# Optimization experiments

Hardware: AMD Instinct MI355X
Metric: run time of the kernel (lower is better)

Reference implementation:

```python
import jax, jax.numpy as jnp
import numpy as np

EPS = 1e-8


def setup_inputs() -> dict:
    key = jax.random.key(0)
    k1, k2 = jax.random.split(key)
    N, F, K, C = 16384, 64, 32, 100
    membership = jax.random.uniform(k1, (N, F, K), dtype=jnp.float32)
    teacher_probs = jax.random.uniform(k2, (N, C), dtype=jnp.float32)
    return {"membership": membership, "teacher_probs": teacher_probs}


def reference(membership, teacher_probs):
    # membership: [N, F, K]  soft bin assignments per feature
    # teacher_probs: [N, C]  teacher class distribution per sample
    N, F, K = membership.shape
    bin_mass = membership.sum(axis=0) + EPS  # [F, K]
    # Contraction form of (membership[:, :, :, None] * teacher_probs[:, None, None, :]).sum(0)
    # avoids the N*F*K*C intermediate.
    centroids = jnp.einsum('nfk,nc->fkc', membership, teacher_probs) / bin_mass[:, :, None]  # [F, K, C]
    # Intra-bin: minimize entropy of each bin's class distribution, mass-weighted.
    intra_entropy = -jnp.sum(centroids * jnp.log(centroids + EPS), axis=2)  # [F, K]
    loss_intra = jnp.sum(intra_entropy * bin_mass) / N
    # Inter-bin: maximize entropy of the mixture of adjacent bins
    # (loss_inter is negative entropy summed, added with +0.5 weight).
    mixture = 0.5 * (centroids[:, :-1, :] + centroids[:, 1:, :])  # [F, K-1, C]
    loss_inter = jnp.sum(mixture * jnp.log(mixture + EPS))
    return loss_intra + 0.5 * loss_inter
```

## Files before the change

kernel.cpp:

```cpp
#include <hip/hip_runtime.h>
#include <hip/hip_bf16.h>

#define NS   16384
#define FKD  2048
#define CD   100
#define CP   112
#define MT   64
#define EPSF 1e-8f
#define SFK  (FKD * CP)
#define NGRP (NS / 8)

typedef float f32x4 __attribute__((ext_vector_type(4)));
typedef short bf16x8 __attribute__((ext_vector_type(8)));

__device__ inline unsigned short f2bf(float f) {
    unsigned int u = __float_as_uint(f);
    u += 0x7FFFu + ((u >> 16) & 1u);
    return (unsigned short)(u >> 16);
}

__global__ __launch_bounds__(256) void ebl_prep(
    const float* __restrict__ tp, unsigned short* __restrict__ Bp)
{
    const int idx = blockIdx.x * 256 + threadIdx.x;
    if (idx >= NGRP * CP) return;
    const int g = idx / CP, c = idx - g * CP;
    unsigned short v[8];
    if (c < CD) {
        const float* p = tp + (size_t)g * 8 * CD + c;
        #pragma unroll
        for (int j = 0; j < 8; ++j) v[j] = f2bf(p[(size_t)j * CD]);
    } else {
        const unsigned short fill = (c == CD) ? 0x3F80 : 0;
        #pragma unroll
        for (int j = 0; j < 8; ++j) v[j] = fill;
    }
    *reinterpret_cast<uint4*>(Bp + (size_t)idx * 8) = *reinterpret_cast<const uint4*>(v);
}

__global__ __launch_bounds__(256, 4) void ebl_gemm(
    const float* __restrict__ mem, const unsigned short* __restrict__ Bp,
    float* __restrict__ spart, int steps)
{
    const int t  = threadIdx.x;
    const int w  = t >> 6;
    const int l  = t & 63;
    const int lg = l >> 4, lr = l & 15;
    const int m  = blockIdx.x * MT + w * 16 + lr;
    const int kc = blockIdx.y;
    const int g0 = kc * steps * 4 + lg;

    const float*          ap = mem + (size_t)g0 * 8 * FKD + m;
    const unsigned short* bp = Bp + ((size_t)g0 * CP + lr) * 8;

    f32x4 acc[7];
    #pragma unroll
    for (int i = 0; i < 7; ++i) acc[i] = (f32x4){0.f, 0.f, 0.f, 0.f};

    float  aC[8]; bf16x8 bC[7];
    #pragma unroll
    for (int j = 0; j < 8; ++j) aC[j] = ap[(size_t)j * FKD];
    #pragma unroll
    for (int nt = 0; nt < 7; ++nt)
        bC[nt] = *reinterpret_cast<const bf16x8*>(bp + nt * 128);

    for (int s = 0; s < steps - 1; ++s) {
        const float*          ap2 = ap + (size_t)32 * FKD;
        const unsigned short* bp2 = bp + 4 * CP * 8;
        float  aN[8]; bf16x8 bN[7];
        #pragma unroll
        for (int j = 0; j < 8; ++j) aN[j] = ap2[(size_t)j * FKD];
        #pragma unroll
        for (int nt = 0; nt < 7; ++nt)
            bN[nt] = *reinterpret_cast<const bf16x8*>(bp2 + nt * 128);

        bf16x8 af;
        #pragma unroll
        for (int j = 0; j < 8; ++j) af[j] = (short)f2bf(aC[j]);
        #pragma unroll
        for (int nt = 0; nt < 7; ++nt)
            acc[nt] = __builtin_amdgcn_mfma_f32_16x16x32_bf16(af, bC[nt], acc[nt], 0, 0, 0);

        ap = ap2; bp = bp2;
        #pragma unroll
        for (int j = 0; j < 8; ++j) aC[j] = aN[j];
        #pragma unroll
        for (int nt = 0; nt < 7; ++nt) bC[nt] = bN[nt];
    }
    {
        bf16x8 af;
        #pragma unroll
        for (int j = 0; j < 8; ++j) af[j] = (short)f2bf(aC[j]);
        #pragma unroll
        for (int nt = 0; nt < 7; ++nt)
            acc[nt] = __builtin_amdgcn_mfma_f32_16x16x32_bf16(af, bC[nt], acc[nt], 0, 0, 0);
    }

    float* sp = spart + (size_t)kc * SFK;
    #pragma unroll
    for (int nt = 0; nt < 7; ++nt) {
        const int c = nt * 16 + lr;
        #pragma unroll
        for (int r = 0; r < 4; ++r) {
            const int mm = blockIdx.x * MT + w * 16 + lg * 4 + r;
            sp[(size_t)mm * CP + c] = acc[nt][r];
        }
    }
}

__global__ __launch_bounds__(256) void ebl_reduce(
    const float* __restrict__ spart, float* __restrict__ S, int NK)
{
    const int idx = blockIdx.x * 256 + threadIdx.x;
    if (idx >= SFK) return;
    float s = 0.f;
    for (int p = 0; p < NK; ++p) s += spart[(size_t)p * SFK + idx];
    S[idx] = s;
}

__global__ __launch_bounds__(256) void ebl_entropy(
    const float* __restrict__ S, float* __restrict__ fpart)
{
    __shared__ float Ss[32 * CP];
    __shared__ float massL[32];
    __shared__ float red[4];
    const int t = threadIdx.x;
    const int f = blockIdx.x;

    for (int idx = t; idx < 32 * CP; idx += 256)
        Ss[idx] = S[(size_t)f * 32 * CP + idx];
    __syncthreads();
    if (t < 32) massL[t] = Ss[t * CP + CD] + EPSF;
    __syncthreads();

    float a_int = 0.f, a_mix = 0.f;
    for (int idx = t; idx < 32 * CD; idx += 256) {
        const int k = idx / CD, c = idx - k * CD;
        const float cent = Ss[k * CP + c] / massL[k];
        a_int -= cent * logf(cent + EPSF) * massL[k];
    }
    for (int idx = t; idx < 31 * CD; idx += 256) {
        const int k = idx / CD, c = idx - k * CD;
        const float mix = 0.5f * (Ss[k * CP + c] / massL[k] + Ss[(k + 1) * CP + c] / massL[k + 1]);
        a_mix += mix * logf(mix + EPSF);
    }

    float part = a_int * (1.0f / (float)NS) + 0.5f * a_mix;
    #pragma unroll
    for (int off = 32; off > 0; off >>= 1) part += __shfl_down(part, off);
    if ((t & 63) == 0) red[t >> 6] = part;
    __syncthreads();
    if (t == 0) fpart[f] = (red[0] + red[1]) + (red[2] + red[3]);
}

__global__ void ebl_finalize(const float* __restrict__ fpart, float* __restrict__ out) {
    float v = fpart[threadIdx.x];
    #pragma unroll
    for (int off = 32; off > 0; off >>= 1) v += __shfl_down(v, off);
    if (threadIdx.x == 0) out[0] = v;
}

extern "C" void kernel_launch(void* const* d_in, const int* in_sizes, int n_in,
                              void* d_out, int out_size, void* d_ws, size_t ws_size,
                              hipStream_t stream)
{
    const float* mem = (const float*)d_in[0];
    const float* tp  = (const float*)d_in[1];
    float* out = (float*)d_out;

    const size_t bpBytes = (size_t)NGRP * CP * 8 * 2;

    int NK = 32;
    while (NK > 1 && bpBytes + ((size_t)NK * SFK + SFK + 64) * 4 > ws_size) NK >>= 1;
    const int steps = NS / (NK * 32);

    unsigned short* Bp = (unsigned short*)d_ws;
    float* spart = (float*)((char*)d_ws + bpBytes);
    float* S     = spart + (size_t)NK * SFK;
    float* fpart = S + SFK;

    ebl_prep<<<(NGRP * CP + 255) / 256, 256, 0, stream>>>(tp, Bp);
    dim3 grid(FKD / MT, NK);
    ebl_gemm<<<grid, 256, 0, stream>>>(mem, Bp, spart, steps);
    ebl_reduce<<<(SFK + 255) / 256, 256, 0, stream>>>(spart, S, NK);
    ebl_entropy<<<64, 256, 0, stream>>>(S, fpart);
    ebl_finalize<<<1, 64, 0, stream>>>(fpart, out);
}
```

Before: 63.35 us.

## Store split-K partials as bf16, double-buffer GEMM loads with nontemporal reads

The split-K partial sums are now written as bf16 instead of fp32, which halves partial-buffer traffic in both the GEMM epilogue and the reduction. The reduction kernel now reads eight values per thread through a vectorized 16-byte load. The GEMM main loop is unrolled by two with ping-pong register buffers, and membership is read with nontemporal loads. Rounding the partials to bf16 adds precision loss. The loop also assumes steps is even and at least 2.

```diff
diff --git a/kernel.cpp b/kernel.cpp
--- a/kernel.cpp
+++ b/kernel.cpp
@@ -11,6 +11,7 @@
 #define NGRP (NS / 8)
 
 typedef float f32x4 __attribute__((ext_vector_type(4)));
+typedef float f32x8 __attribute__((ext_vector_type(8)));
 typedef short bf16x8 __attribute__((ext_vector_type(8)));
 
 __device__ inline unsigned short f2bf(float f) {
@@ -40,7 +41,7 @@
 
 __global__ __launch_bounds__(256, 4) void ebl_gemm(
     const float* __restrict__ mem, const unsigned short* __restrict__ Bp,
-    float* __restrict__ spart, int steps)
+    unsigned short* __restrict__ spart, int steps)
 {
     const int t  = threadIdx.x;
     const int w  = t >> 6;
@@ -52,70 +53,77 @@
 
     const float*          ap = mem + (size_t)g0 * 8 * FKD + m;
     const unsigned short* bp = Bp + ((size_t)g0 * CP + lr) * 8;
+    const size_t aStep = (size_t)32 * FKD;
+    const size_t bStep = (size_t)4 * CP * 8;
 
     f32x4 acc[7];
     #pragma unroll
     for (int i = 0; i < 7; ++i) acc[i] = (f32x4){0.f, 0.f, 0.f, 0.f};
 
-    float  aC[8]; bf16x8 bC[7];
-    #pragma unroll
-    for (int j = 0; j < 8; ++j) aC[j] = ap[(size_t)j * FKD];
-    #pragma unroll
-    for (int nt = 0; nt < 7; ++nt)
-        bC[nt] = *reinterpret_cast<const bf16x8*>(bp + nt * 128);
+    float a0[8], a1[8]; bf16x8 b0[7], b1[7];
 
-    for (int s = 0; s < steps - 1; ++s) {
-        const float*          ap2 = ap + (size_t)32 * FKD;
-        const unsigned short* bp2 = bp + 4 * CP * 8;
-        float  aN[8]; bf16x8 bN[7];
-        #pragma unroll
-        for (int j = 0; j < 8; ++j) aN[j] = ap2[(size_t)j * FKD];
-        #pragma unroll
-        for (int nt = 0; nt < 7; ++nt)
-            bN[nt] = *reinterpret_cast<const bf16x8*>(bp2 + nt * 128);
+#define LOADA(dst, base) { \
+    const float* _p = (base); \
+    _Pragma("unroll") \
+    for (int j = 0; j < 8; ++j) dst[j] = __builtin_nontemporal_load(_p + (size_t)j * FKD); }
+#define LOADB(dst, base) { \
+    const unsigned short* _q = (base); \
+    _Pragma("unroll") \
+    for (int nt = 0; nt < 7; ++nt) dst[nt] = *reinterpret_cast<const bf16x8*>(_q + nt * 128); }
+#define COMPUTE(aB, bB) { \
+    bf16x8 af; \
+    _Pragma("unroll") \
+    for (int j = 0; j < 8; ++j) af[j] = (short)f2bf(aB[j]); \
+    _Pragma("unroll") \
+    for (int nt = 0; nt < 7; ++nt) \
+        acc[nt] = __builtin_amdgcn_mfma_f32_16x16x32_bf16(af, bB[nt], acc[nt], 0, 0, 0); }
 
-        bf16x8 af;
-        #pragma unroll
-        for (int j = 0; j < 8; ++j) af[j] = (short)f2bf(aC[j]);
-        #pragma unroll
-        for (int nt = 0; nt < 7; ++nt)
-            acc[nt] = __builtin_amdgcn_mfma_f32_16x16x32_bf16(af, bC[nt], acc[nt], 0, 0, 0);
+    LOADA(a0, ap);             LOADB(b0, bp);
+    LOADA(a1, ap + aStep);     LOADB(b1, bp + bStep);
 
-        ap = ap2; bp = bp2;
-        #pragma unroll
-        for (int j = 0; j < 8; ++j) aC[j] = aN[j];
-        #pragma unroll
-        for (int nt = 0; nt < 7; ++nt) bC[nt] = bN[nt];
+    for (int s = 0; s < steps - 2; s += 2) {
+        COMPUTE(a0, b0);
+        LOADA(a0, ap + 2 * aStep);  LOADB(b0, bp + 2 * bStep);
+        COMPUTE(a1, b1);
+        LOADA(a1, ap + 3 * aStep);  LOADB(b1, bp + 3 * bStep);
+        ap += 2 * aStep; bp += 2 * bStep;
     }
-    {
-        bf16x8 af;
-        #pragma unroll
-        for (int j = 0; j < 8; ++j) af[j] = (short)f2bf(aC[j]);
-        #pragma unroll
-        for (int nt = 0; nt < 7; ++nt)
-            acc[nt] = __builtin_amdgcn_mfma_f32_16x16x32_bf16(af, bC[nt], acc[nt], 0, 0, 0);
-    }
+    COMPUTE(a0, b0);
+    COMPUTE(a1, b1);
 
-    float* sp = spart + (size_t)kc * SFK;
+#undef LOADA
+#undef LOADB
+#undef COMPUTE
+
+    unsigned short* sp = spart + (size_t)kc * SFK;
     #pragma unroll
     for (int nt = 0; nt < 7; ++nt) {
         const int c = nt * 16 + lr;
         #pragma unroll
         for (int r = 0; r < 4; ++r) {
             const int mm = blockIdx.x * MT + w * 16 + lg * 4 + r;
-            sp[(size_t)mm * CP + c] = acc[nt][r];
+            sp[(size_t)mm * CP + c] = f2bf(acc[nt][r]);
         }
     }
 }
 
 __global__ __launch_bounds__(256) void ebl_reduce(
-    const float* __restrict__ spart, float* __restrict__ S, int NK)
+    const unsigned short* __restrict__ spart, float* __restrict__ S, int NK)
 {
-    const int idx = blockIdx.x * 256 + threadIdx.x;
-    if (idx >= SFK) return;
-    float s = 0.f;
-    for (int p = 0; p < NK; ++p) s += spart[(size_t)p * SFK + idx];
-    S[idx] = s;
+    const int v = blockIdx.x * 256 + threadIdx.x;
+    if (v >= SFK / 8) return;
+    float s[8];
+    #pragma unroll
+    for (int j = 0; j < 8; ++j) s[j] = 0.f;
+    for (int p = 0; p < NK; ++p) {
+        uint4 raw = *reinterpret_cast<const uint4*>(spart + (size_t)p * SFK + (size_t)v * 8);
+        const unsigned short* u = reinterpret_cast<const unsigned short*>(&raw);
+        #pragma unroll
+        for (int j = 0; j < 8; ++j) s[j] += __uint_as_float((unsigned)u[j] << 16);
+    }
+    f32x4* out = reinterpret_cast<f32x4*>(S + (size_t)v * 8);
+    out[0] = (f32x4){s[0], s[1], s[2], s[3]};
+    out[1] = (f32x4){s[4], s[5], s[6], s[7]};
 }
 
 __global__ __launch_bounds__(256) void ebl_entropy(
@@ -171,18 +179,19 @@
     const size_t bpBytes = (size_t)NGRP * CP * 8 * 2;
 
     int NK = 32;
-    while (NK > 1 && bpBytes + ((size_t)NK * SFK + SFK + 64) * 4 > ws_size) NK >>= 1;
+    while (NK > 1 &&
+           bpBytes + (size_t)NK * SFK * 2 + ((size_t)SFK + 64) * 4 > ws_size) NK >>= 1;
     const int steps = NS / (NK * 32);
 
-    unsigned short* Bp = (unsigned short*)d_ws;
-    float* spart = (float*)((char*)d_ws + bpBytes);
-    float* S     = spart + (size_t)NK * SFK;
-    float* fpart = S + SFK;
+    unsigned short* Bp    = (unsigned short*)d_ws;
+    unsigned short* spart = (unsigned short*)((char*)d_ws + bpBytes);
+    float*          S     = (float*)((char*)spart + (size_t)NK * SFK * 2);
+    float*          fpart = S + SFK;
 
     ebl_prep<<<(NGRP * CP + 255) / 256, 256, 0, stream>>>(tp, Bp);
     dim3 grid(FKD / MT, NK);
     ebl_gemm<<<grid, 256, 0, stream>>>(mem, Bp, spart, steps);
-    ebl_reduce<<<(SFK + 255) / 256, 256, 0, stream>>>(spart, S, NK);
+    ebl_reduce<<<(SFK / 8 + 255) / 256, 256, 0, stream>>>(spart, S, NK);
     ebl_entropy<<<64, 256, 0, stream>>>(S, fpart);
     ebl_finalize<<<1, 64, 0, stream>>>(fpart, out);
 }
```

New measurement: 94.95 us. +49.9%, slower.
